# Kernel optimization log

Measured on AMD Instinct MI355X. Metric: run time of the kernel, lower is better.

## Reference

```python
import jax, jax.numpy as jnp
import numpy as np

B, S, V, H, L, NH, DH, F = 1, 512, 30522, 768, 12, 12, 64, 3072
N, E, GH, NC = 50000, 800000, 128, 3


def setup_inputs() -> dict:
    key = jax.random.key(0)
    ks = iter(jax.random.split(key, 48))
    def nrm(shape, s=0.02):
        return jax.random.normal(next(ks), shape, jnp.float32) * s
    inp = {
        "input_ids": jax.random.randint(next(ks), (B, S), 0, V, dtype=jnp.int32),
        "attention_mask": jnp.ones((B, S), jnp.int32),
        "token_type_ids": jnp.zeros((B, S), jnp.int32),
        "premise_edge_index": jax.random.randint(next(ks), (2, E), 0, N, dtype=jnp.int32),
        "hypothesis_edge_index": jax.random.randint(next(ks), (2, E), 0, N, dtype=jnp.int32),
        "premise_node_features": nrm((N, H), 1.0),
        "hypothesis_node_features": nrm((N, H), 1.0),
        "word_emb": nrm((V, H)), "pos_emb": nrm((S, H)), "type_emb": nrm((2, H)),
        "emb_ln_s": jnp.ones((H,)), "emb_ln_b": jnp.zeros((H,)),
        "Wq": nrm((L, H, H)), "bq": jnp.zeros((L, H)),
        "Wk": nrm((L, H, H)), "bk": jnp.zeros((L, H)),
        "Wv": nrm((L, H, H)), "bv": jnp.zeros((L, H)),
        "Wo": nrm((L, H, H)), "bo": jnp.zeros((L, H)),
        "ln1_s": jnp.ones((L, H)), "ln1_b": jnp.zeros((L, H)),
        "W1": nrm((L, H, F)), "b1": jnp.zeros((L, F)),
        "W2": nrm((L, F, H)), "b2": jnp.zeros((L, H)),
        "ln2_s": jnp.ones((L, H)), "ln2_b": jnp.zeros((L, H)),
        "gcn_W1": nrm((H, GH), 0.05), "gcn_b1": jnp.zeros((GH,)),
        "gcn_W2": nrm((GH, GH), 0.05), "gcn_b2": jnp.zeros((GH,)),
        "comb_W": nrm((2 * (H + GH), H)), "comb_b": jnp.zeros((H,)),
        "cls_W": nrm((H, NC)), "cls_b": jnp.zeros((NC,)),
    }
    return inp


def _ln(x, s, b, eps=1e-12):
    m = jnp.mean(x, -1, keepdims=True)
    v = jnp.mean(jnp.square(x - m), -1, keepdims=True)
    return (x - m) * jax.lax.rsqrt(v + eps) * s + b


def _gcn(x, edge_index, W1, b1, W2, b2):
    # PyG GCNConv: add self-loops, symmetric D^-1/2 A D^-1/2 normalization,
    # linear transform first, then scatter-add messages at destination.
    n = x.shape[0]
    loops = jnp.arange(n, dtype=edge_index.dtype)
    src = jnp.concatenate([edge_index[0], loops])
    dst = jnp.concatenate([edge_index[1], loops])
    deg = jax.ops.segment_sum(jnp.ones(src.shape[0], jnp.float32), dst, num_segments=n)
    dinv = jnp.where(deg > 0, jax.lax.rsqrt(jnp.maximum(deg, 1e-12)), 0.0)
    norm = (dinv[src] * dinv[dst])[:, None]
    def conv(h, W, b):
        hw = h @ W
        return jax.ops.segment_sum(hw[src] * norm, dst, num_segments=n) + b
    h = jax.nn.relu(conv(x, W1, b1))
    h = conv(h, W2, b2)
    # global_mean_pool with batch=None -> single graph mean, shape [1, GH]
    return jnp.mean(h, axis=0, keepdims=True)


def _bert(input_ids, attention_mask, token_type_ids, word_emb, pos_emb, type_emb, emb_ln_s, emb_ln_b, layer_params):
    s = input_ids.shape[1]
    h = word_emb[input_ids] + pos_emb[None, :s] + type_emb[token_type_ids]
    h = _ln(h, emb_ln_s, emb_ln_b)
    bias = (1.0 - attention_mask.astype(jnp.float32))[:, None, None, :] * -1e4
    def step(h, p):
        wq, bq, wk, bk, wv, bv, wo, bo, l1s, l1b, w1, b1_, w2, b2_, l2s, l2b = p
        b_, s_, _ = h.shape
        q = (h @ wq + bq).reshape(b_, s_, NH, DH)
        k = (h @ wk + bk).reshape(b_, s_, NH, DH)
        v = (h @ wv + bv).reshape(b_, s_, NH, DH)
        scores = jnp.einsum('bqhd,bkhd->bhqk', q, k) / np.float32(np.sqrt(DH)) + bias
        ctx = jnp.einsum('bhqk,bkhd->bqhd', jax.nn.softmax(scores, -1), v).reshape(b_, s_, H)
        h1 = _ln(h + ctx @ wo + bo, l1s, l1b)
        f = jax.nn.gelu(h1 @ w1 + b1_, approximate=False) @ w2 + b2_
        return _ln(h1 + f, l2s, l2b), None
    h, _ = jax.lax.scan(step, h, layer_params)
    return h[:, 0, :]  # CLS pooling, [B, H]


def reference(input_ids, attention_mask, token_type_ids, premise_edge_index, premise_node_features, hypothesis_edge_index, hypothesis_node_features, word_emb, pos_emb, type_emb, emb_ln_s, emb_ln_b, Wq, bq, Wk, bk, Wv, bv, Wo, bo, ln1_s, ln1_b, W1, b1, W2, b2, ln2_s, ln2_b, gcn_W1, gcn_b1, gcn_W2, gcn_b2, comb_W, comb_b, cls_W, cls_b):
    lp = (Wq, bq, Wk, bk, Wv, bv, Wo, bo, ln1_s, ln1_b, W1, b1, W2, b2, ln2_s, ln2_b)
    cls = _bert(input_ids, attention_mask, token_type_ids, word_emb, pos_emb, type_emb, emb_ln_s, emb_ln_b, lp)
    gp = _gcn(premise_node_features, premise_edge_index, gcn_W1, gcn_b1, gcn_W2, gcn_b2)
    gh = _gcn(hypothesis_node_features, hypothesis_edge_index, gcn_W1, gcn_b1, gcn_W2, gcn_b2)
    cp = jnp.concatenate([cls, gp], -1)
    ch = jnp.concatenate([cls, gh], -1)
    fc = jnp.concatenate([cp, ch], -1)  # [1, 2*(H+GH)]
    feat = jax.nn.relu(fc @ comb_W + comb_b)  # dropout is identity at eval
    return feat @ cls_W + cls_b
```

## Files before the change

kernel.cpp:

```cpp
#include <hip/hip_runtime.h>
#include <math.h>

constexpr int kS = 512, kH = 768, kNH = 12, kDH = 64, kF = 3072, kL = 12;
constexpr int kN = 50000, kE = 800000, kGH = 128;

#define CDIV(a,b) (((a)+(b)-1)/(b))

struct Ptr3 { const float* p[3]; };

typedef __attribute__((ext_vector_type(8))) short bf16x8;
typedef __attribute__((ext_vector_type(4))) float f32x4;

__device__ __forceinline__ unsigned short bf16_rne(float f) {
    unsigned int u = __float_as_uint(f);
    u += 0x7fffu + ((u >> 16) & 1u);
    return (unsigned short)(u >> 16);
}
__device__ __forceinline__ float bf16_f32(unsigned short h) {
    return __uint_as_float(((unsigned int)h) << 16);
}
__device__ __forceinline__ void split2(float f, short& hi, short& lo) {
    unsigned short h = bf16_rne(f);
    hi = (short)h;
    lo = (short)bf16_rne(f - bf16_f32(h));
// ... 122 lines not shown
        for (int j = 0; j < 4; j++) acc[i][j] = (f32x4){0.f, 0.f, 0.f, 0.f};
    int nst = Kc / 32;
    bf16x8 pa0 = *(const bf16x8*)(Agh);
    bf16x8 pa1 = *(const bf16x8*)(Agl);
    bf16x8 pb0 = *(const bf16x8*)(Bgh);
    bf16x8 pb1 = *(const bf16x8*)(Bgh + 8);
    bf16x8 pb2 = *(const bf16x8*)(Bgl);
    bf16x8 pb3 = *(const bf16x8*)(Bgl + 8);
    for (int st = 0; st < nst; ++st) {
        *(bf16x8*)&As[aofs]      = pa0;
        *(bf16x8*)&As[aofs + 32] = pa1;
        *(bf16x8*)&Bs[bofs]      = pb0;
        *(bf16x8*)&Bs[bofs + 8]  = pb1;
        *(bf16x8*)&Bs[bofs + 32] = pb2;
        *(bf16x8*)&Bs[bofs + 40] = pb3;
        if (st + 1 < nst) {
            int go = (st + 1) * 32;
            pa0 = *(const bf16x8*)(Agh + go);
            pa1 = *(const bf16x8*)(Agl + go);
            pb0 = *(const bf16x8*)(Bgh + go);
            pb1 = *(const bf16x8*)(Bgh + go + 8);
            pb2 = *(const bf16x8*)(Bgl + go);
            pb3 = *(const bf16x8*)(Bgl + go + 8);
        }
        __syncthreads();
        bf16x8 bh[4], bl[4];
        #pragma unroll
        for (int j = 0; j < 4; j++) {
            int c = (wn + j * 16 + fr) * LDR + ko;
            bh[j] = *(const bf16x8*)&Bs[c];
            bl[j] = *(const bf16x8*)&Bs[c + 32];
        }
        #pragma unroll
        for (int i = 0; i < 2; i++) {
            int r = (wm + i * 16 + fr) * LDR + ko;
            bf16x8 ah = *(const bf16x8*)&As[r];
            bf16x8 al = *(const bf16x8*)&As[r + 32];
            #pragma unroll
            for (int j = 0; j < 4; j++) {
                acc[i][j] = __builtin_amdgcn_mfma_f32_16x16x32_bf16(ah, bh[j], acc[i][j], 0, 0, 0);
                acc[i][j] = __builtin_amdgcn_mfma_f32_16x16x32_bf16(ah, bl[j], acc[i][j], 0, 0, 0);
                acc[i][j] = __builtin_amdgcn_mfma_f32_16x16x32_bf16(al, bh[j], acc[i][j], 0, 0, 0);
            }
        }
        __syncthreads();
    }
    long MN = (long)M * Nn;
    float* Pp = part + (long)(w * S + s) * MN;
    int cr = (lane >> 4) * 4;
    #pragma unroll
    for (int i = 0; i < 2; i++) {
        #pragma unroll
        for (int r = 0; r < 4; r++) {
            int gm = m0 + wm + i * 16 + cr + r;
            float* rowp = &Pp[(long)gm * Nn + n0 + wn + fr];
            #pragma unroll
            for (int j = 0; j < 4; j++) rowp[j * 16] = acc[i][j][r];
        }
    }
}

__global__ __launch_bounds__(256, 4) void gemm64_gcn(
    const float* __restrict__ A,
    const short* __restrict__ Bth, const short* __restrict__ Btl,
    float* __restrict__ part, int M, int Nn, int K, int S)
{
    __shared__ short As[64 * LDR], Bs[128 * LDR];
    int s = blockIdx.z;
    int Kc = K / S, kbeg = s * Kc;
    int m0 = blockIdx.y * 64, n0 = blockIdx.x * 128;
    int tid = threadIdx.x;
    int ar = tid >> 2, aqf = (tid & 3) * 8;
    int gmA = m0 + ar; if (gmA > M - 1) gmA = M - 1;
    const float* Agf = A + (long)gmA * K + kbeg + aqf;
    int aofs = ar * LDR + aqf;
    int br = tid >> 1, bq = (tid & 1) * 16;
    const short* Bgh = Bth + (long)(n0 + br) * K + kbeg + bq;
    const short* Bgl = Btl + (long)(n0 + br) * K + kbeg + bq;
    int bofs = br * LDR + bq;
    int wid = tid >> 6, lane = tid & 63;
    int wm = (wid >> 1) * 32, wn = (wid & 1) * 64;
    int fr = lane & 15, ko = (lane >> 4) * 8;
    f32x4 acc[2][4];
    #pragma unroll
    for (int i = 0; i < 2; i++)
        #pragma unroll
        for (int j = 0; j < 4; j++) acc[i][j] = (f32x4){0.f, 0.f, 0.f, 0.f};
    int nst = Kc / 32;
    float4 pf0 = *(const float4*)(Agf);
    float4 pf1 = *(const float4*)(Agf + 4);
    bf16x8 pb0 = *(const bf16x8*)(Bgh);
    bf16x8 pb1 = *(const bf16x8*)(Bgh + 8);
    bf16x8 pb2 = *(const bf16x8*)(Bgl);
    bf16x8 pb3 = *(const bf16x8*)(Bgl + 8);
    for (int st = 0; st < nst; ++st) {
        short h0, l0, h1, l1, h2, l2, h3, l3, h4, l4, h5, l5, h6, l6, h7, l7;
        split2(pf0.x, h0, l0); split2(pf0.y, h1, l1); split2(pf0.z, h2, l2); split2(pf0.w, h3, l3);
        split2(pf1.x, h4, l4); split2(pf1.y, h5, l5); split2(pf1.z, h6, l6); split2(pf1.w, h7, l7);
        *(short4*)&As[aofs]      = make_short4(h0, h1, h2, h3);
        *(short4*)&As[aofs + 4]  = make_short4(h4, h5, h6, h7);
        *(short4*)&As[aofs + 32] = make_short4(l0, l1, l2, l3);
        *(short4*)&As[aofs + 36] = make_short4(l4, l5, l6, l7);
        *(bf16x8*)&Bs[bofs]      = pb0;
        *(bf16x8*)&Bs[bofs + 8]  = pb1;
        *(bf16x8*)&Bs[bofs + 32] = pb2;
        *(bf16x8*)&Bs[bofs + 40] = pb3;
        if (st + 1 < nst) {
            int go = (st + 1) * 32;
            pf0 = *(const float4*)(Agf + go);
            pf1 = *(const float4*)(Agf + go + 4);
            pb0 = *(const bf16x8*)(Bgh + go);
            pb1 = *(const bf16x8*)(Bgh + go + 8);
            pb2 = *(const bf16x8*)(Bgl + go);
            pb3 = *(const bf16x8*)(Bgl + go + 8);
        }
        __syncthreads();
        bf16x8 bh[4], bl[4];
        #pragma unroll
        for (int j = 0; j < 4; j++) {
            int c = (wn + j * 16 + fr) * LDR + ko;
            bh[j] = *(const bf16x8*)&Bs[c];
            bl[j] = *(const bf16x8*)&Bs[c + 32];
        }
        #pragma unroll
        for (int i = 0; i < 2; i++) {
            int r = (wm + i * 16 + fr) * LDR + ko;
            bf16x8 ah = *(const bf16x8*)&As[r];
            bf16x8 al = *(const bf16x8*)&As[r + 32];
            #pragma unroll
            for (int j = 0; j < 4; j++) {
                acc[i][j] = __builtin_amdgcn_mfma_f32_16x16x32_bf16(ah, bh[j], acc[i][j], 0, 0, 0);
                acc[i][j] = __builtin_amdgcn_mfma_f32_16x16x32_bf16(ah, bl[j], acc[i][j], 0, 0, 0);
                acc[i][j] = __builtin_amdgcn_mfma_f32_16x16x32_bf16(al, bh[j], acc[i][j], 0, 0, 0);
            }
        }
        __syncthreads();
    }
    long MN = (long)M * Nn;
    float* Pp = part + (long)s * MN;
    int cr = (lane >> 4) * 4;
    #pragma unroll
    for (int i = 0; i < 2; i++) {
        #pragma unroll
        for (int r = 0; r < 4; r++) {
            int gm = m0 + wm + i * 16 + cr + r;
            if (gm >= M) continue;
            float* rowp = &Pp[(long)gm * Nn + n0 + wn + fr];
            #pragma unroll
            for (int j = 0; j < 4; j++) rowp[j * 16] = acc[i][j][r];
        }
    }
}

__global__ void splitk_epi_qkv_kernel(const float* __restrict__ part, Ptr3 bias,
                                      short* __restrict__ qh, short* __restrict__ ql,
                                      short* __restrict__ kh, short* __restrict__ kl,
                                      short* __restrict__ vh, short* __restrict__ vl,
                                      int S) {
    const long MN = (long)kS * kH;
    int w = blockIdx.y;
    long i = ((long)blockIdx.x * blockDim.x + threadIdx.x) * 4;
    if (i >= MN) return;
    const float* P = part + (long)w * S * MN + i;
    float4 a = *(const float4*)P;
    for (int s2 = 1; s2 < S; ++s2) {
        float4 b2 = *(const float4*)(P + (long)s2 * MN);
        a.x += b2.x; a.y += b2.y; a.z += b2.z; a.w += b2.w;
    }
    const float* bw = bias.p[w];
    int n = (int)(i % kH);
    a.x += bw[n]; a.y += bw[n + 1]; a.z += bw[n + 2]; a.w += bw[n + 3];
    short* oh = (w == 0) ? qh : (w == 1) ? kh : vh;
    short* ol = (w == 0) ? ql : (w == 1) ? kl : vl;
    short h0, l0, h1, l1, h2, l2, h3, l3;
    split2(a.x, h0, l0); split2(a.y, h1, l1); split2(a.z, h2, l2); split2(a.w, h3, l3);
    *(short4*)&oh[i] = make_short4(h0, h1, h2, h3);
    *(short4*)&ol[i] = make_short4(l0, l1, l2, l3);
}

__global__ void splitk_epi_sh_kernel(const float* __restrict__ part, const float* __restrict__ bias,
                                     short* __restrict__ oh, short* __restrict__ ol,
                                     long MN, int Nn, int S, int act) {
    long i = ((long)blockIdx.x * blockDim.x + threadIdx.x) * 4;
    if (i >= MN) return;
    const float* P = part + i;
    float4 a = *(const float4*)P;
    for (int s2 = 1; s2 < S; ++s2) {
        float4 b2 = *(const float4*)(P + (long)s2 * MN);
        a.x += b2.x; a.y += b2.y; a.z += b2.z; a.w += b2.w;
    }
    if (bias) {
        int n = (int)(i % Nn);
        a.x += bias[n]; a.y += bias[n + 1]; a.z += bias[n + 2]; a.w += bias[n + 3];
    }
    if (act == 1) {
        a.x = 0.5f * a.x * (1.f + erff(a.x * 0.70710678118654752f));
        a.y = 0.5f * a.y * (1.f + erff(a.y * 0.70710678118654752f));
        a.z = 0.5f * a.z * (1.f + erff(a.z * 0.70710678118654752f));
        a.w = 0.5f * a.w * (1.f + erff(a.w * 0.70710678118654752f));
    }
    short h0, l0, h1, l1, h2, l2, h3, l3;
    split2(a.x, h0, l0); split2(a.y, h1, l1); split2(a.z, h2, l2); split2(a.w, h3, l3);
    *(short4*)&oh[i] = make_short4(h0, h1, h2, h3);
    *(short4*)&ol[i] = make_short4(l0, l1, l2, l3);
}

__global__ void splitk_epi_ln2_kernel(const float* __restrict__ part, const float* __restrict__ bias,
                                      const float* __restrict__ res, const float* __restrict__ g,
                                      const float* __restrict__ b, float* __restrict__ out,
                                      short* __restrict__ oh, short* __restrict__ ol, int S) {
    int row = blockIdx.x; int tid = threadIdx.x;
    __shared__ float red[256];
    const long MN = (long)kS * kH;
    float vals[3]; float sum = 0.f;
    #pragma unroll
    for (int r = 0; r < 3; r++) {
        int j = tid + r * 256;
        const float* P = part + (long)row * kH + j;
        float x = res[(long)row * kH + j] + bias[j];
        for (int s2 = 0; s2 < S; ++s2) x += P[(long)s2 * MN];
        vals[r] = x; sum += x;
    }
    red[tid] = sum; __syncthreads();
    for (int off = 128; off > 0; off >>= 1) { if (tid < off) red[tid] += red[tid + off]; __syncthreads(); }
    float mean = red[0] / kH; __syncthreads();
    float vs = 0.f;
    #pragma unroll
    for (int r = 0; r < 3; r++) { float d = vals[r] - mean; vs += d * d; }
    red[tid] = vs; __syncthreads();
    for (int off = 128; off > 0; off >>= 1) { if (tid < off) red[tid] += red[tid + off]; __syncthreads(); }
    float rstd = rsqrtf(red[0] / kH + 1e-12f);
    #pragma unroll
    for (int r = 0; r < 3; r++) {
        int j = tid + r * 256;
        float o = (vals[r] - mean) * rstd * g[j] + b[j];
        out[(long)row * kH + j] = o;
        short hi, lo; split2(o, hi, lo);
        oh[(long)row * kH + j] = hi; ol[(long)row * kH + j] = lo;
    }
}

__global__ __launch_bounds__(256, 4) void attn_scores64_kernel(
    const short* __restrict__ qh, const short* __restrict__ ql,
    const short* __restrict__ kh, const short* __restrict__ kl,
    const float* __restrict__ mb, float* __restrict__ scores)
{
    __shared__ short As[64 * LDR], Bs[128 * LDR];
    int h = blockIdx.z;
    int k0 = blockIdx.x * 128, q0 = blockIdx.y * 64;
    int tid = threadIdx.x;
    int ar = tid >> 2, aq = (tid & 3) * 8;
    const short* Agh = qh + (long)(q0 + ar) * kH + h * kDH + aq;
    const short* Agl = ql + (long)(q0 + ar) * kH + h * kDH + aq;
    int aofs = ar * LDR + aq;
    int br = tid >> 1, bq = (tid & 1) * 16;
    const short* Bgh = kh + (long)(k0 + br) * kH + h * kDH + bq;
    const short* Bgl = kl + (long)(k0 + br) * kH + h * kDH + bq;
    int bofs = br * LDR + bq;
    int wid = tid >> 6, lane = tid & 63;
    int wm = (wid >> 1) * 32, wn = (wid & 1) * 64;
    int fr = lane & 15, ko = (lane >> 4) * 8;
    f32x4 acc[2][4];
    #pragma unroll
    for (int i = 0; i < 2; i++)
        #pragma unroll
        for (int j = 0; j < 4; j++) acc[i][j] = (f32x4){0.f, 0.f, 0.f, 0.f};
    bf16x8 pa0 = *(const bf16x8*)(Agh);
    bf16x8 pa1 = *(const bf16x8*)(Agl);
    bf16x8 pb0 = *(const bf16x8*)(Bgh);
    bf16x8 pb1 = *(const bf16x8*)(Bgh + 8);
    bf16x8 pb2 = *(const bf16x8*)(Bgl);
    bf16x8 pb3 = *(const bf16x8*)(Bgl + 8);
    #pragma unroll
    for (int st = 0; st < 2; ++st) {
        *(bf16x8*)&As[aofs]      = pa0;
        *(bf16x8*)&As[aofs + 32] = pa1;
        *(bf16x8*)&Bs[bofs]      = pb0;
        *(bf16x8*)&Bs[bofs + 8]  = pb1;
        *(bf16x8*)&Bs[bofs + 32] = pb2;
        *(bf16x8*)&Bs[bofs + 40] = pb3;
        if (st == 0) {
            pa0 = *(const bf16x8*)(Agh + 32);
            pa1 = *(const bf16x8*)(Agl + 32);
            pb0 = *(const bf16x8*)(Bgh + 32);
            pb1 = *(const bf16x8*)(Bgh + 40);
            pb2 = *(const bf16x8*)(Bgl + 32);
            pb3 = *(const bf16x8*)(Bgl + 40);
        }
        __syncthreads();
        bf16x8 bh[4], bl[4];
        #pragma unroll
        for (int j = 0; j < 4; j++) {
            int c = (wn + j * 16 + fr) * LDR + ko;
            bh[j] = *(const bf16x8*)&Bs[c];
            bl[j] = *(const bf16x8*)&Bs[c + 32];
        }
        #pragma unroll
        for (int i = 0; i < 2; i++) {
            int r = (wm + i * 16 + fr) * LDR + ko;
            bf16x8 ah = *(const bf16x8*)&As[r];
            bf16x8 al = *(const bf16x8*)&As[r + 32];
            #pragma unroll
            for (int j = 0; j < 4; j++) {
                acc[i][j] = __builtin_amdgcn_mfma_f32_16x16x32_bf16(ah, bh[j], acc[i][j], 0, 0, 0);
                acc[i][j] = __builtin_amdgcn_mfma_f32_16x16x32_bf16(ah, bl[j], acc[i][j], 0, 0, 0);
                acc[i][j] = __builtin_amdgcn_mfma_f32_16x16x32_bf16(al, bh[j], acc[i][j], 0, 0, 0);
            }
        }
        __syncthreads();
    }
    int cr = (lane >> 4) * 4;
    #pragma unroll
    for (int i = 0; i < 2; i++) {
        #pragma unroll
        for (int r = 0; r < 4; r++) {
            int qq = q0 + wm + i * 16 + cr + r;
            float* rowp = &scores[((long)h * kS + qq) * kS + k0 + wn + fr];
            #pragma unroll
            for (int j = 0; j < 4; j++)
                rowp[j * 16] = acc[i][j][r] * 0.125f + mb[k0 + wn + j * 16 + fr];
        }
    }
}

__global__ void softmax_split_kernel(const float* __restrict__ scores,
                                     short* __restrict__ ph, short* __restrict__ pl) {
    long row = blockIdx.x;
    const float* p = scores + row * kS;
    int tid = threadIdx.x;
    __shared__ float red[256];
    float x0 = p[tid], x1 = p[tid + 256];
    red[tid] = fmaxf(x0, x1); __syncthreads();
    for (int off = 128; off > 0; off >>= 1) { if (tid < off) red[tid] = fmaxf(red[tid], red[tid + off]); __syncthreads(); }
    float mx = red[0]; __syncthreads();
    float e0 = expf(x0 - mx), e1 = expf(x1 - mx);
    red[tid] = e0 + e1; __syncthreads();
    for (int off = 128; off > 0; off >>= 1) { if (tid < off) red[tid] += red[tid + off]; __syncthreads(); }
    float inv = 1.f / red[0];
    float r0 = e0 * inv, r1 = e1 * inv;
    short h0, l0, h1, l1;
    split2(r0, h0, l0); split2(r1, h1, l1);
    ph[row * kS + tid] = h0; pl[row * kS + tid] = l0;
    ph[row * kS + tid + 256] = h1; pl[row * kS + tid + 256] = l1;
}

__global__ __launch_bounds__(256, 4) void attn_ctx64_kernel(
    const short* __restrict__ ph, const short* __restrict__ pl,
    const short* __restrict__ vth, const short* __restrict__ vtl,
    float* __restrict__ part)
{
    __shared__ short As[128 * LDR], Bs[64 * LDR];
    int q0 = blockIdx.x * 128;
    int h = blockIdx.y >> 3, s = blockIdx.y & 7;
    int kbeg = s * 64;
    int tid = threadIdx.x;
    int ar = tid >> 1, aq = (tid & 1) * 16;
    const short* Agh = ph + ((long)h * kS + q0 + ar) * kS + kbeg + aq;
    const short* Agl = pl + ((long)h * kS + q0 + ar) * kS + kbeg + aq;
    int aofs = ar * LDR + aq;
    int brr = tid >> 2, bq = (tid & 3) * 8;
    const short* Bgh = vth + ((long)h * kDH + brr) * kS + kbeg + bq;
    const short* Bgl = vtl + ((long)h * kDH + brr) * kS + kbeg + bq;
    int bofs = brr * LDR + bq;
    int wid = tid >> 6, lane = tid & 63;
    int wm = wid * 32;
    int fr = lane & 15, ko = (lane >> 4) * 8;
    f32x4 acc[2][4];
    #pragma unroll
    for (int i = 0; i < 2; i++)
        #pragma unroll
        for (int j = 0; j < 4; j++) acc[i][j] = (f32x4){0.f, 0.f, 0.f, 0.f};
    bf16x8 pa0 = *(const bf16x8*)(Agh);
    bf16x8 pa1 = *(const bf16x8*)(Agh + 8);
    bf16x8 pa2 = *(const bf16x8*)(Agl);
    bf16x8 pa3 = *(const bf16x8*)(Agl + 8);
    bf16x8 pb0 = *(const bf16x8*)(Bgh);
    bf16x8 pb1 = *(const bf16x8*)(Bgl);
    #pragma unroll
    for (int st = 0; st < 2; ++st) {
        *(bf16x8*)&As[aofs]      = pa0;
        *(bf16x8*)&As[aofs + 8]  = pa1;
        *(bf16x8*)&As[aofs + 32] = pa2;
        *(bf16x8*)&As[aofs + 40] = pa3;
        *(bf16x8*)&Bs[bofs]      = pb0;
        *(bf16x8*)&Bs[bofs + 32] = pb1;
        if (st == 0) {
            pa0 = *(const bf16x8*)(Agh + 32);
            pa1 = *(const bf16x8*)(Agh + 40);
            pa2 = *(const bf16x8*)(Agl + 32);
            pa3 = *(const bf16x8*)(Agl + 40);
            pb0 = *(const bf16x8*)(Bgh + 32);
            pb1 = *(const bf16x8*)(Bgl + 32);
        }
        __syncthreads();
        bf16x8 bh[4], bl[4];
        #pragma unroll
        for (int j = 0; j < 4; j++) {
            int c = (j * 16 + fr) * LDR + ko;
            bh[j] = *(const bf16x8*)&Bs[c];
            bl[j] = *(const bf16x8*)&Bs[c + 32];
        }
        #pragma unroll
        for (int i = 0; i < 2; i++) {
            int r = (wm + i * 16 + fr) * LDR + ko;
            bf16x8 ah = *(const bf16x8*)&As[r];
            bf16x8 al = *(const bf16x8*)&As[r + 32];
            #pragma unroll
            for (int j = 0; j < 4; j++) {
                acc[i][j] = __builtin_amdgcn_mfma_f32_16x16x32_bf16(ah, bh[j], acc[i][j], 0, 0, 0);
                acc[i][j] = __builtin_amdgcn_mfma_f32_16x16x32_bf16(ah, bl[j], acc[i][j], 0, 0, 0);
                acc[i][j] = __builtin_amdgcn_mfma_f32_16x16x32_bf16(al, bh[j], acc[i][j], 0, 0, 0);
            }
        }
        __syncthreads();
    }
    long Pbase = (long)s * ((long)kS * kH);
    int cr = (lane >> 4) * 4;
    #pragma unroll
    for (int i = 0; i < 2; i++) {
        #pragma unroll
        for (int r = 0; r < 4; r++) {
            int gq = q0 + wm + i * 16 + cr + r;
            float* rowp = &part[Pbase + (long)gq * kH + h * kDH + fr];
            #pragma unroll
            for (int j = 0; j < 4; j++) rowp[j * 16] = acc[i][j][r];
        }
    }
}

__global__ void cnt_kernel(const int* __restrict__ dst, int* __restrict__ cnt, int E) {
    int e = blockIdx.x * blockDim.x + threadIdx.x;
    if (e < E) atomicAdd(&cnt[dst[e]], 1);
}

__global__ void scan1_kernel(const int* __restrict__ cnt, int* __restrict__ offs,
                             int* __restrict__ bsum, int n) {
    __shared__ int sh[256];
    int i = blockIdx.x * 256 + threadIdx.x;
    int v = (i < n) ? cnt[i] : 0;
    sh[threadIdx.x] = v; __syncthreads();
    for (int off = 1; off < 256; off <<= 1) {
        int t = (threadIdx.x >= off) ? sh[threadIdx.x - off] : 0;
        __syncthreads();
        sh[threadIdx.x] += t;
        __syncthreads();
    }
    if (i < n) offs[i] = sh[threadIdx.x] - v;
    if (threadIdx.x == 255) bsum[blockIdx.x] = sh[255];
}

__global__ void scan2_kernel(int* bsum, int nb, int* offs, int n) {
    if (threadIdx.x == 0) {
        int run = 0;
        for (int b = 0; b < nb; b++) { int t = bsum[b]; bsum[b] = run; run += t; }
        offs[n] = run;
    }
}

__global__ void scan3_kernel(const int* __restrict__ cnt, int* __restrict__ offs,
                             const int* __restrict__ bsum, int* __restrict__ cur,
                             float* __restrict__ dinv, int n) {
    int i = blockIdx.x * 256 + threadIdx.x;
    if (i >= n) return;
    int o = offs[i] + bsum[blockIdx.x];
    offs[i] = o; cur[i] = o;
    dinv[i] = rsqrtf((float)(cnt[i] + 1));
}

__global__ void csrfill_edgew_kernel(const int* __restrict__ src, const int* __restrict__ dst,
                                     int* __restrict__ cur, int* __restrict__ csr,
                                     const float* __restrict__ dinv, float* __restrict__ wsum,
                                     int E) {
    int e = blockIdx.x * blockDim.x + threadIdx.x;
    if (e < E) {
        int s2 = src[e], d = dst[e];
        int slot = atomicAdd(&cur[d], 1);
        csr[slot] = s2;
        atomicAdd(&wsum[s2], dinv[s2] * dinv[d]);
    }
}

__global__ __launch_bounds__(256) void spmm_gather_kernel(const int* __restrict__ offs,
                                                          const int* __restrict__ csr,
                                                          const float* __restrict__ dinv,
                                                          const float* __restrict__ hw,
                                                          const float* __restrict__ b1,
                                                          float* __restrict__ hout, int n) {
    int d = blockIdx.x * 2 + (threadIdx.x >> 7);
    int j = threadIdx.x & 127;
    if (d >= n) return;
    int beg = offs[d], end = offs[d + 1];
    float a0 = 0.f, a1 = 0.f, a2 = 0.f, a3 = 0.f;
    int p = beg;
    for (; p + 4 <= end; p += 4) {
        int s0 = csr[p], s1 = csr[p + 1], s2 = csr[p + 2], s3 = csr[p + 3];
        a0 += dinv[s0] * hw[(long)s0 * kGH + j];
        a1 += dinv[s1] * hw[(long)s1 * kGH + j];
        a2 += dinv[s2] * hw[(long)s2 * kGH + j];
        a3 += dinv[s3] * hw[(long)s3 * kGH + j];
    }
    for (; p < end; ++p) {
        int s4 = csr[p];
        a0 += dinv[s4] * hw[(long)s4 * kGH + j];
    }
    float acc = (a0 + a1) + (a2 + a3);
    float dd = dinv[d];
    float v = acc * dd + dd * dd * hw[(long)d * kGH + j] + b1[j];
    hout[(long)d * kGH + j] = fmaxf(v, 0.f);
}

__global__ void wreduce_kernel(const float* __restrict__ h, const float* __restrict__ w,
                               const float* __restrict__ dinv, float* __restrict__ s, int n) {
    int tid = threadIdx.x; int j = tid & 127; int half = tid >> 7;
    float acc = 0.f;
    for (int u = blockIdx.x * 2 + half; u < n; u += gridDim.x * 2) {
        float di = dinv[u];
        acc += (w[u] + di * di) * h[(long)u * kGH + j];
    }
    __shared__ float red[256];
    red[tid] = acc; __syncthreads();
    if (tid < 128) atomicAdd(&s[j], red[tid] + red[tid + 128]);
}

__global__ void gcn_final_kernel(const float* s, const float* W2, const float* b2, float* g) {
    int j2 = threadIdx.x;
    float acc = 0.f;
    for (int j = 0; j < kGH; j++) acc += s[j] * W2[(long)j * kGH + j2];
    g[j2] = acc * (1.f / (float)kN) + b2[j2];
}

__global__ void combine_part_kernel(const float* __restrict__ cls, const float* __restrict__ gp,
                                    const float* __restrict__ gh, const float* __restrict__ Wc,
                                    float* __restrict__ feat) {
    int i0 = blockIdx.x * 32;
    int tid = threadIdx.x;
    float a0 = 0.f, a1 = 0.f, a2 = 0.f;
    for (int r = 0; r < 32; r++) {
        int i = i0 + r;
        float x = (i < 768) ? cls[i] : (i < 896) ? gp[i - 768]
                : (i < 1664) ? cls[i - 896] : gh[i - 1664];
        const float* row = Wc + (long)i * kH;
        a0 += x * row[tid]; a1 += x * row[tid + 256]; a2 += x * row[tid + 512];
    }
    atomicAdd(&feat[tid], a0);
    atomicAdd(&feat[tid + 256], a1);
    atomicAdd(&feat[tid + 512], a2);
}

__global__ void combine_fin_kernel(float* feat, const float* bc) {
    int o = blockIdx.x * 256 + threadIdx.x;
    if (o < kH) feat[o] = fmaxf(feat[o] + bc[o], 0.f);
}

__global__ void cls_head_kernel(const float* feat, const float* W, const float* b, float* out) {
    int tid = threadIdx.x;
    float a0 = 0.f, a1 = 0.f, a2 = 0.f;
    for (int o = tid; o < kH; o += 256) {
        float f = feat[o];
        a0 += f * W[o * 3 + 0]; a1 += f * W[o * 3 + 1]; a2 += f * W[o * 3 + 2];
    }
    __shared__ float r0[256], r1[256], r2[256];
    r0[tid] = a0; r1[tid] = a1; r2[tid] = a2; __syncthreads();
    for (int off = 128; off > 0; off >>= 1) {
        if (tid < off) { r0[tid] += r0[tid + off]; r1[tid] += r1[tid + off]; r2[tid] += r2[tid + off]; }
        __syncthreads();
    }
    if (tid == 0) { out[0] = r0[0] + b[0]; out[1] = r1[0] + b[1]; out[2] = r2[0] + b[2]; }
}

extern "C" void kernel_launch(void* const* d_in, const int* in_sizes, int n_in,
                              void* d_out, int out_size, void* d_ws, size_t ws_size,
                              hipStream_t stream) {
    const int*   input_ids = (const int*)d_in[0];
    const int*   attn_mask = (const int*)d_in[1];
    const int*   type_ids  = (const int*)d_in[2];
    const int*   p_edges   = (const int*)d_in[3];
    const int*   h_edges   = (const int*)d_in[4];
    const float* p_nodes   = (const float*)d_in[5];
    const float* h_nodes   = (const float*)d_in[6];
    const float* word_emb  = (const float*)d_in[7];
    const float* pos_emb   = (const float*)d_in[8];
    const float* type_emb  = (const float*)d_in[9];
    const float* eln_s     = (const float*)d_in[10];
    const float* eln_b     = (const float*)d_in[11];
    const float* Wq = (const float*)d_in[12]; const float* bq = (const float*)d_in[13];
    const float* Wk = (const float*)d_in[14]; const float* bk = (const float*)d_in[15];
    const float* Wv = (const float*)d_in[16]; const float* bv = (const float*)d_in[17];
    const float* Wo = (const float*)d_in[18]; const float* bo = (const float*)d_in[19];
    const float* l1s = (const float*)d_in[20]; const float* l1b = (const float*)d_in[21];
    const float* W1 = (const float*)d_in[22]; const float* b1 = (const float*)d_in[23];
    const float* W2 = (const float*)d_in[24]; const float* b2 = (const float*)d_in[25];
    const float* l2s = (const float*)d_in[26]; const float* l2b = (const float*)d_in[27];
    const float* gW1 = (const float*)d_in[28]; const float* gb1 = (const float*)d_in[29];
    const float* gW2 = (const float*)d_in[30]; const float* gb2 = (const float*)d_in[31];
    const float* cW  = (const float*)d_in[32]; const float* cb  = (const float*)d_in[33];
    const float* clsW = (const float*)d_in[34]; const float* clsB = (const float*)d_in[35];
    float* out = (float*)d_out;

    float* W = (float*)d_ws;
    size_t off = 0;
    auto alloc = [&](size_t n) { float* p = W + off; off += n; return p; };
    float* h    = alloc((size_t)kS * kH);
    float* h1   = alloc((size_t)kS * kH);
    float* deg  = alloc(kN);
    float* wsum = alloc(kN);
    float* svec = alloc(kGH);
    float* gp   = alloc(kGH);
    float* ghv  = alloc(kGH);
    float* mb   = alloc(kS);
    float* feat = alloc(kH);
    float* big  = W + off;

    float* part  = big;
    float* scores = part;
    short* p_h   = (short*)(big + 4718592);
    short* p_l   = p_h + (size_t)3145728;
    short* ffn1_h = (short*)(big + 7864320);
    short* ffn1_l = ffn1_h + (size_t)1572864;
    short* sm    = (short*)(big + 11796480);
    const size_t SMN = (size_t)kS * kH;
    short* q_h = sm;            short* q_l = q_h + SMN;
    short* k_h = q_l + SMN;     short* k_l = k_h + SMN;
    short* v_h = k_l + SMN;     short* v_l = v_h + SMN;
    short* vt_h = v_l + SMN;    short* vt_l = vt_h + SMN;
    short* ctx_h = vt_l + SMN;  short* ctx_l = ctx_h + SMN;
    short* h1_h = ctx_l + SMN;  short* h1_l = h1_h + SMN;
    short* hh_h = h1_l + SMN;   short* hh_l = hh_h + SMN;

    float* hw1 = big;
    float* agg = big + (size_t)kN * kGH;
    int* icnt  = (int*)(big + 2 * (size_t)kN * kGH);
    int* ioffs = icnt + 50048;
    int* icur  = ioffs + 50048;
    int* ibsum = icur + 50048;
    int* icsr  = ibsum + 256;
    short* gwt_h = (short*)(icsr + kE);
    short* gwt_l = gwt_h + (size_t)kH * kGH;

    const size_t QKV_SZ = (size_t)kH * kH;
    const size_t FF_SZ  = (size_t)kH * kF;
    short* wc = (short*)(big + 15000000);
    short* qkv_h = wc;                          short* qkv_l = qkv_h + 12 * 3 * QKV_SZ;
    short* wo_h  = qkv_l + 12 * 3 * QKV_SZ;     short* wo_l  = wo_h + 12 * QKV_SZ;
    short* w1_h  = wo_l + 12 * QKV_SZ;          short* w1_l  = w1_h + 12 * FF_SZ;
    short* w2_h  = w1_l + 12 * FF_SZ;           short* w2_l  = w2_h + 12 * FF_SZ;

    const long MN_H = (long)kS * kH;
    const long MN_F = (long)kS * kF;
    const int nScanBlk = CDIV(kN, 256);

    wtrans_all_kernel<<<dim3(24, 24, 12), 256, 0, stream>>>(Wq, qkv_h,              qkv_l,              kH, kH, (long)(3 * QKV_SZ));
    wtrans_all_kernel<<<dim3(24, 24, 12), 256, 0, stream>>>(Wk, qkv_h + QKV_SZ,     qkv_l + QKV_SZ,     kH, kH, (long)(3 * QKV_SZ));
    wtrans_all_kernel<<<dim3(24, 24, 12), 256, 0, stream>>>(Wv, qkv_h + 2 * QKV_SZ, qkv_l + 2 * QKV_SZ, kH, kH, (long)(3 * QKV_SZ));
    wtrans_all_kernel<<<dim3(24, 24, 12), 256, 0, stream>>>(Wo, wo_h, wo_l, kH, kH, (long)QKV_SZ);
    wtrans_all_kernel<<<dim3(96, 24, 12), 256, 0, stream>>>(W1, w1_h, w1_l, kH, kF, (long)FF_SZ);
    wtrans_all_kernel<<<dim3(24, 96, 12), 256, 0, stream>>>(W2, w2_h, w2_l, kF, kH, (long)FF_SZ);

    const int* gsrc[2] = { p_edges, h_edges };
    const int* gdst[2] = { p_edges + kE, h_edges + kE };
    const float* gx[2] = { p_nodes, h_nodes };
    float* gout[2] = { gp, ghv };
    wtrans_all_kernel<<<dim3(kGH / 32, kH / 32, 1), 256, 0, stream>>>(gW1, gwt_h, gwt_l, kH, kGH, 0);
    for (int gi = 0; gi < 2; gi++) {
        gcn_zero_kernel<<<nScanBlk, 256, 0, stream>>>(icnt, wsum, svec);
        cnt_kernel<<<CDIV(kE, 256), 256, 0, stream>>>(gdst[gi], icnt, kE);
        scan1_kernel<<<nScanBlk, 256, 0, stream>>>(icnt, ioffs, ibsum, kN);
        scan2_kernel<<<1, 64, 0, stream>>>(ibsum, nScanBlk, ioffs, kN);
        scan3_kernel<<<nScanBlk, 256, 0, stream>>>(icnt, ioffs, ibsum, icur, deg, kN);
        csrfill_edgew_kernel<<<CDIV(kE, 256), 256, 0, stream>>>(
            gsrc[gi], gdst[gi], icur, icsr, deg, wsum, kE);
        gemm64_gcn<<<dim3(1, CDIV(kN, 64), 1), 256, 0, stream>>>(
            gx[gi], gwt_h, gwt_l, hw1, kN, kGH, kH, 1);
        spmm_gather_kernel<<<CDIV(kN, 2), 256, 0, stream>>>(ioffs, icsr, deg, hw1, gb1, agg, kN);
        wreduce_kernel<<<512, 256, 0, stream>>>(agg, wsum, deg, svec, kN);
        gcn_final_kernel<<<1, kGH, 0, stream>>>(svec, gW2, gb2, gout[gi]);
    }

    embed_ln_kernel<<<kS, 256, 0, stream>>>(input_ids, type_ids, attn_mask,
                                            word_emb, pos_emb, type_emb,
                                            eln_s, eln_b, h, hh_h, hh_l, mb);
    for (int l = 0; l < kL; l++) {
        const float* bq_l = bq + (size_t)l * kH;
        const float* bk_l = bk + (size_t)l * kH;
        const float* bv_l = bv + (size_t)l * kH;
        const float* bo_l = bo + (size_t)l * kH;
        const float* b1_l = b1 + (size_t)l * kF;
        const float* b2_l = b2 + (size_t)l * kH;
        const float* l1s_l = l1s + (size_t)l * kH; const float* l1b_l = l1b + (size_t)l * kH;
        const float* l2s_l = l2s + (size_t)l * kH; const float* l2b_l = l2b + (size_t)l * kH;
        const short* qkvh_l = qkv_h + (size_t)l * 3 * QKV_SZ;
        const short* qkvl_l = qkv_l + (size_t)l * 3 * QKV_SZ;
        const short* woh_l = wo_h + (size_t)l * QKV_SZ;
        const short* wol_l = wo_l + (size_t)l * QKV_SZ;
        const short* w1h_l = w1_h + (size_t)l * FF_SZ;
        const short* w1l_l = w1_l + (size_t)l * FF_SZ;
        const short* w2h_l = w2_h + (size_t)l * FF_SZ;
        const short* w2l_l = w2_l + (size_t)l * FF_SZ;

        gemm64_pre<<<dim3(kH / 128, kS / 64, 12), 256, 0, stream>>>(
            hh_h, hh_l, qkvh_l, qkvl_l, (long)QKV_SZ, part, kS, kH, kH, 4);
        splitk_epi_qkv_kernel<<<dim3((int)(MN_H / 4 / 256), 3), 256, 0, stream>>>(
            part, Ptr3{{bq_l, bk_l, bv_l}}, q_h, q_l, k_h, k_l, v_h, v_l, 4);
        vtrans_kernel<<<dim3(kS / 32, kNH * 2), 256, 0, stream>>>(v_h, v_l, vt_h, vt_l);
        attn_scores64_kernel<<<dim3(kS / 128, kS / 64, kNH), 256, 0, stream>>>(
            q_h, q_l, k_h, k_l, mb, scores);
        softmax_split_kernel<<<kNH * kS, 256, 0, stream>>>(scores, p_h, p_l);
        attn_ctx64_kernel<<<dim3(kS / 128, kNH * 8), 256, 0, stream>>>(p_h, p_l, vt_h, vt_l, part);
        splitk_epi_sh_kernel<<<(int)(MN_H / 4 / 256), 256, 0, stream>>>(
            part, nullptr, ctx_h, ctx_l, MN_H, kH, 8, 0);
        gemm64_pre<<<dim3(kH / 128, kS / 64, 8), 256, 0, stream>>>(
            ctx_h, ctx_l, woh_l, wol_l, 0, part, kS, kH, kH, 8);
        splitk_epi_ln2_kernel<<<kS, 256, 0, stream>>>(part, bo_l, h, l1s_l, l1b_l, h1, h1_h, h1_l, 8);
        gemm64_pre<<<dim3(kF / 128, kS / 64, 4), 256, 0, stream>>>(
            h1_h, h1_l, w1h_l, w1l_l, 0, part, kS, kF, kH, 4);
        splitk_epi_sh_kernel<<<(int)(MN_F / 4 / 256), 256, 0, stream>>>(
            part, b1_l, ffn1_h, ffn1_l, MN_F, kF, 4, 1);
        gemm64_pre<<<dim3(kH / 128, kS / 64, 8), 256, 0, stream>>>(
            ffn1_h, ffn1_l, w2h_l, w2l_l, 0, part, kS, kH, kF, 8);
        splitk_epi_ln2_kernel<<<kS, 256, 0, stream>>>(part, b2_l, h1, l2s_l, l2b_l, h, hh_h, hh_l, 8);
    }

    fill_kernel<<<3, 256, 0, stream>>>(feat, 0.f, kH);
    combine_part_kernel<<<56, 256, 0, stream>>>(h, gp, ghv, cW, feat);
    combine_fin_kernel<<<3, 256, 0, stream>>>(feat, cb);
    cls_head_kernel<<<1, 256, 0, stream>>>(feat, clsW, clsB, out);
}
```

Before: 2.454 ms.

## Fuse attention scores, softmax, and context into one flash-attention kernel

Replaces the separate score GEMM, softmax, context GEMM and split-K epilogue with a single online-softmax flash attention kernel per 64-query tile and head. This removes the fp32 score buffer and the split bf16 probability buffers and their round trips through global memory, plus three launches per layer. The cost is a small grid (96 blocks of 128 threads), serialized K/V tile loads with many barriers, and a sequential split of the unnormalized probabilities into hi and lo passes, which can leave the GPU underused. Separately, the GCN aggregation loop is unrolled from 4 to 8 accumulators to expose more memory-level parallelism.

```diff
diff --git a/kernel.cpp b/kernel.cpp
--- a/kernel.cpp
+++ b/kernel.cpp
@@ -298,6 +298,219 @@
     }
 }
 
+__global__ __launch_bounds__(128) void flash_attn_kernel(
+    const short* __restrict__ qh, const short* __restrict__ ql,
+    const short* __restrict__ kh, const short* __restrict__ kl,
+    const short* __restrict__ vth, const short* __restrict__ vtl,
+    const float* __restrict__ mb,
+    short* __restrict__ ctxh, short* __restrict__ ctxl)
+{
+    __shared__ short Qs[2 * 64 * LDR];
+    __shared__ short Ks[128 * LDR];
+    __shared__ short Ps[4 * 64 * 40];
+    int h = blockIdx.y;
+    int q0 = blockIdx.x * 64;
+    int tid = threadIdx.x;
+    int wid = tid >> 6, lane = tid & 63;
+    int wm = wid * 32;
+    int fr = lane & 15, ko = (lane >> 4) * 8;
+    int cr4 = (lane >> 4) * 4;
+    {
+        int row = tid >> 1, dseg = tid & 1;
+        const short* gh_ = qh + (long)(q0 + row) * kH + h * kDH + dseg * 32;
+        const short* gl_ = ql + (long)(q0 + row) * kH + h * kDH + dseg * 32;
+        short* dst = &Qs[(dseg * 64 + row) * LDR];
+        #pragma unroll
+        for (int c = 0; c < 4; c++) {
+            *(bf16x8*)&dst[c * 8]      = *(const bf16x8*)(gh_ + c * 8);
+            *(bf16x8*)&dst[32 + c * 8] = *(const bf16x8*)(gl_ + c * 8);
+        }
+    }
+    float mrun[2][4], lrun[2][4];
+    f32x4 accO[2][4];
+    #pragma unroll
+    for (int i = 0; i < 2; i++)
+        #pragma unroll
+        for (int r = 0; r < 4; r++) { mrun[i][r] = -1e30f; lrun[i][r] = 0.f; }
+    #pragma unroll
+    for (int i = 0; i < 2; i++)
+        #pragma unroll
+        for (int j = 0; j < 4; j++) accO[i][j] = (f32x4){0.f, 0.f, 0.f, 0.f};
+
+    for (int t = 0; t < 4; ++t) {
+        int k0t = t * 128;
+        f32x4 accS[2][8];
+        #pragma unroll
+        for (int i = 0; i < 2; i++)
+            #pragma unroll
+            for (int j = 0; j < 8; j++) accS[i][j] = (f32x4){0.f, 0.f, 0.f, 0.f};
+        for (int st = 0; st < 2; ++st) {
+            __syncthreads();
+            {
+                int row = tid;
+                const short* gh_ = kh + (long)(k0t + row) * kH + h * kDH + st * 32;
+                const short* gl_ = kl + (long)(k0t + row) * kH + h * kDH + st * 32;
+                short* dst = &Ks[row * LDR];
+                #pragma unroll
+                for (int c = 0; c < 4; c++) {
+                    *(bf16x8*)&dst[c * 8]      = *(const bf16x8*)(gh_ + c * 8);
+                    *(bf16x8*)&dst[32 + c * 8] = *(const bf16x8*)(gl_ + c * 8);
+                }
+            }
+            __syncthreads();
+            bf16x8 bh[8], bl[8];
+            #pragma unroll
+            for (int j = 0; j < 8; j++) {
+                int c = (j * 16 + fr) * LDR + ko;
+                bh[j] = *(const bf16x8*)&Ks[c];
+                bl[j] = *(const bf16x8*)&Ks[c + 32];
+            }
+            #pragma unroll
+            for (int i = 0; i < 2; i++) {
+                int r = (st * 64 + wm + i * 16 + fr) * LDR + ko;
+                bf16x8 ah = *(const bf16x8*)&Qs[r];
+                bf16x8 al = *(const bf16x8*)&Qs[r + 32];
+                #pragma unroll
+                for (int j = 0; j < 8; j++) {
+                    accS[i][j] = __builtin_amdgcn_mfma_f32_16x16x32_bf16(ah, bh[j], accS[i][j], 0, 0, 0);
+                    accS[i][j] = __builtin_amdgcn_mfma_f32_16x16x32_bf16(ah, bl[j], accS[i][j], 0, 0, 0);
+                    accS[i][j] = __builtin_amdgcn_mfma_f32_16x16x32_bf16(al, bh[j], accS[i][j], 0, 0, 0);
+                }
+            }
+        }
+        float mbv[8];
+        #pragma unroll
+        for (int j = 0; j < 8; j++) mbv[j] = mb[k0t + j * 16 + fr];
+        #pragma unroll
+        for (int i = 0; i < 2; i++) {
+            #pragma unroll
+            for (int r = 0; r < 4; r++) {
+                float mt = -1e30f;
+                #pragma unroll
+                for (int j = 0; j < 8; j++) {
+                    float sv = accS[i][j][r] * 0.125f + mbv[j];
+                    accS[i][j][r] = sv;
+                    mt = fmaxf(mt, sv);
+                }
+                #pragma unroll
+                for (int mmask = 1; mmask < 16; mmask <<= 1)
+                    mt = fmaxf(mt, __shfl_xor(mt, mmask, 64));
+                float mn = fmaxf(mrun[i][r], mt);
+                float sc = __expf(mrun[i][r] - mn);
+                mrun[i][r] = mn;
+                lrun[i][r] *= sc;
+                #pragma unroll
+                for (int jo = 0; jo < 4; jo++) {
+                    accO[i][jo][r] *= sc;
+                }
+                float lt = 0.f;
+                #pragma unroll
+                for (int j = 0; j < 8; j++) {
+                    float p = __expf(accS[i][j][r] - mn);
+                    accS[i][j][r] = p;
+                    lt += p;
+                }
+                #pragma unroll
+                for (int mmask = 1; mmask < 16; mmask <<= 1)
+                    lt += __shfl_xor(lt, mmask, 64);
+                lrun[i][r] += lt;
+            }
+        }
+        #pragma unroll
+        for (int i = 0; i < 2; i++)
+            #pragma unroll
+            for (int j = 0; j < 8; j++)
+                #pragma unroll
+                for (int r = 0; r < 4; r++) {
+                    int rowp = wm + i * 16 + cr4 + r;
+                    Ps[(j >> 1) * 2560 + rowp * 40 + (j & 1) * 16 + fr] =
+                        (short)bf16_rne(accS[i][j][r]);
+                }
+        for (int st2 = 0; st2 < 4; ++st2) {
+            __syncthreads();
+            {
+                int row = tid >> 1, half = tid & 1;
+                const short* gh_ = vth + ((long)h * kDH + row) * kS + k0t + st2 * 32 + half * 16;
+                const short* gl_ = vtl + ((long)h * kDH + row) * kS + k0t + st2 * 32 + half * 16;
+                short* dst = &Ks[row * LDR + half * 16];
+                *(bf16x8*)&dst[0]  = *(const bf16x8*)(gh_);
+                *(bf16x8*)&dst[8]  = *(const bf16x8*)(gh_ + 8);
+                *(bf16x8*)&dst[32] = *(const bf16x8*)(gl_);
+                *(bf16x8*)&dst[40] = *(const bf16x8*)(gl_ + 8);
+            }
+            __syncthreads();
+            bf16x8 vh_[4], vl_[4];
+            #pragma unroll
+            for (int j = 0; j < 4; j++) {
+                int c = (j * 16 + fr) * LDR + ko;
+                vh_[j] = *(const bf16x8*)&Ks[c];
+                vl_[j] = *(const bf16x8*)&Ks[c + 32];
+            }
+            #pragma unroll
+            for (int i = 0; i < 2; i++) {
+                bf16x8 pa = *(const bf16x8*)&Ps[st2 * 2560 + (wm + i * 16 + fr) * 40 + ko];
+                #pragma unroll
+                for (int j = 0; j < 4; j++) {
+                    accO[i][j] = __builtin_amdgcn_mfma_f32_16x16x32_bf16(pa, vh_[j], accO[i][j], 0, 0, 0);
+                    accO[i][j] = __builtin_amdgcn_mfma_f32_16x16x32_bf16(pa, vl_[j], accO[i][j], 0, 0, 0);
+                }
+            }
+        }
+        __syncthreads();
+        #pragma unroll
+        for (int i = 0; i < 2; i++)
+            #pragma unroll
+            for (int j = 0; j < 8; j++)
+                #pragma unroll
+                for (int r = 0; r < 4; r++) {
+                    int rowp = wm + i * 16 + cr4 + r;
+                    float p = accS[i][j][r];
+                    unsigned short ph = bf16_rne(p);
+                    Ps[(j >> 1) * 2560 + rowp * 40 + (j & 1) * 16 + fr] =
+                        (short)bf16_rne(p - bf16_f32(ph));
+                }
+        for (int st2 = 0; st2 < 4; ++st2) {
+            __syncthreads();
+            {
+                int row = tid >> 1, half = tid & 1;
+                const short* gh_ = vth + ((long)h * kDH + row) * kS + k0t + st2 * 32 + half * 16;
+                short* dst = &Ks[row * LDR + half * 16];
+                *(bf16x8*)&dst[0] = *(const bf16x8*)(gh_);
+                *(bf16x8*)&dst[8] = *(const bf16x8*)(gh_ + 8);
+            }
+            __syncthreads();
+            bf16x8 vh_[4];
+            #pragma unroll
+            for (int j = 0; j < 4; j++)
+                vh_[j] = *(const bf16x8*)&Ks[(j * 16 + fr) * LDR + ko];
+            #pragma unroll
+            for (int i = 0; i < 2; i++) {
+                bf16x8 pa = *(const bf16x8*)&Ps[st2 * 2560 + (wm + i * 16 + fr) * 40 + ko];
+                #pragma unroll
+                for (int j = 0; j < 4; j++)
+                    accO[i][j] = __builtin_amdgcn_mfma_f32_16x16x32_bf16(pa, vh_[j], accO[i][j], 0, 0, 0);
+            }
+        }
+        __syncthreads();
+    }
+    #pragma unroll
+    for (int i = 0; i < 2; i++) {
+        #pragma unroll
+        for (int r = 0; r < 4; r++) {
+            float inv = 1.f / lrun[i][r];
+            int q = q0 + wm + i * 16 + cr4 + r;
+            #pragma unroll
+            for (int j = 0; j < 4; j++) {
+                float o = accO[i][j][r] * inv;
+                int col = h * kDH + j * 16 + fr;
+                short hi, lo; split2(o, hi, lo);
+                ctxh[(long)q * kH + col] = hi;
+                ctxl[(long)q * kH + col] = lo;
+            }
+        }
+    }
+}
+
 __global__ void splitk_epi_qkv_kernel(const float* __restrict__ part, Ptr3 bias,
                                       short* __restrict__ qh, short* __restrict__ ql,
                                       short* __restrict__ kh, short* __restrict__ kl,
@@ -386,194 +599,6 @@
     }
 }
 
-__global__ __launch_bounds__(256, 4) void attn_scores64_kernel(
-    const short* __restrict__ qh, const short* __restrict__ ql,
-    const short* __restrict__ kh, const short* __restrict__ kl,
-    const float* __restrict__ mb, float* __restrict__ scores)
-{
-    __shared__ short As[64 * LDR], Bs[128 * LDR];
-    int h = blockIdx.z;
-    int k0 = blockIdx.x * 128, q0 = blockIdx.y * 64;
-    int tid = threadIdx.x;
-    int ar = tid >> 2, aq = (tid & 3) * 8;
-    const short* Agh = qh + (long)(q0 + ar) * kH + h * kDH + aq;
-    const short* Agl = ql + (long)(q0 + ar) * kH + h * kDH + aq;
-    int aofs = ar * LDR + aq;
-    int br = tid >> 1, bq = (tid & 1) * 16;
-    const short* Bgh = kh + (long)(k0 + br) * kH + h * kDH + bq;
-    const short* Bgl = kl + (long)(k0 + br) * kH + h * kDH + bq;
-    int bofs = br * LDR + bq;
-    int wid = tid >> 6, lane = tid & 63;
-    int wm = (wid >> 1) * 32, wn = (wid & 1) * 64;
-    int fr = lane & 15, ko = (lane >> 4) * 8;
-    f32x4 acc[2][4];
-    #pragma unroll
-    for (int i = 0; i < 2; i++)
-        #pragma unroll
-        for (int j = 0; j < 4; j++) acc[i][j] = (f32x4){0.f, 0.f, 0.f, 0.f};
-    bf16x8 pa0 = *(const bf16x8*)(Agh);
-    bf16x8 pa1 = *(const bf16x8*)(Agl);
-    bf16x8 pb0 = *(const bf16x8*)(Bgh);
-    bf16x8 pb1 = *(const bf16x8*)(Bgh + 8);
-    bf16x8 pb2 = *(const bf16x8*)(Bgl);
-    bf16x8 pb3 = *(const bf16x8*)(Bgl + 8);
-    #pragma unroll
-    for (int st = 0; st < 2; ++st) {
-        *(bf16x8*)&As[aofs]      = pa0;
-        *(bf16x8*)&As[aofs + 32] = pa1;
-        *(bf16x8*)&Bs[bofs]      = pb0;
-        *(bf16x8*)&Bs[bofs + 8]  = pb1;
-        *(bf16x8*)&Bs[bofs + 32] = pb2;
-        *(bf16x8*)&Bs[bofs + 40] = pb3;
-        if (st == 0) {
-            pa0 = *(const bf16x8*)(Agh + 32);
-            pa1 = *(const bf16x8*)(Agl + 32);
-            pb0 = *(const bf16x8*)(Bgh + 32);
-            pb1 = *(const bf16x8*)(Bgh + 40);
-            pb2 = *(const bf16x8*)(Bgl + 32);
-            pb3 = *(const bf16x8*)(Bgl + 40);
-        }
-        __syncthreads();
-        bf16x8 bh[4], bl[4];
-        #pragma unroll
-        for (int j = 0; j < 4; j++) {
-            int c = (wn + j * 16 + fr) * LDR + ko;
-            bh[j] = *(const bf16x8*)&Bs[c];
-            bl[j] = *(const bf16x8*)&Bs[c + 32];
-        }
-        #pragma unroll
-        for (int i = 0; i < 2; i++) {
-            int r = (wm + i * 16 + fr) * LDR + ko;
-            bf16x8 ah = *(const bf16x8*)&As[r];
-            bf16x8 al = *(const bf16x8*)&As[r + 32];
-            #pragma unroll
-            for (int j = 0; j < 4; j++) {
-                acc[i][j] = __builtin_amdgcn_mfma_f32_16x16x32_bf16(ah, bh[j], acc[i][j], 0, 0, 0);
-                acc[i][j] = __builtin_amdgcn_mfma_f32_16x16x32_bf16(ah, bl[j], acc[i][j], 0, 0, 0);
-                acc[i][j] = __builtin_amdgcn_mfma_f32_16x16x32_bf16(al, bh[j], acc[i][j], 0, 0, 0);
-            }
-        }
-        __syncthreads();
-    }
-    int cr = (lane >> 4) * 4;
-    #pragma unroll
-    for (int i = 0; i < 2; i++) {
-        #pragma unroll
-        for (int r = 0; r < 4; r++) {
-            int qq = q0 + wm + i * 16 + cr + r;
-            float* rowp = &scores[((long)h * kS + qq) * kS + k0 + wn + fr];
-            #pragma unroll
-            for (int j = 0; j < 4; j++)
-                rowp[j * 16] = acc[i][j][r] * 0.125f + mb[k0 + wn + j * 16 + fr];
-        }
-    }
-}
-
-__global__ void softmax_split_kernel(const float* __restrict__ scores,
-                                     short* __restrict__ ph, short* __restrict__ pl) {
-    long row = blockIdx.x;
-    const float* p = scores + row * kS;
-    int tid = threadIdx.x;
-    __shared__ float red[256];
-    float x0 = p[tid], x1 = p[tid + 256];
-    red[tid] = fmaxf(x0, x1); __syncthreads();
-    for (int off = 128; off > 0; off >>= 1) { if (tid < off) red[tid] = fmaxf(red[tid], red[tid + off]); __syncthreads(); }
-    float mx = red[0]; __syncthreads();
-    float e0 = expf(x0 - mx), e1 = expf(x1 - mx);
-    red[tid] = e0 + e1; __syncthreads();
-    for (int off = 128; off > 0; off >>= 1) { if (tid < off) red[tid] += red[tid + off]; __syncthreads(); }
-    float inv = 1.f / red[0];
-    float r0 = e0 * inv, r1 = e1 * inv;
-    short h0, l0, h1, l1;
-    split2(r0, h0, l0); split2(r1, h1, l1);
-    ph[row * kS + tid] = h0; pl[row * kS + tid] = l0;
-    ph[row * kS + tid + 256] = h1; pl[row * kS + tid + 256] = l1;
-}
-
-__global__ __launch_bounds__(256, 4) void attn_ctx64_kernel(
-    const short* __restrict__ ph, const short* __restrict__ pl,
-    const short* __restrict__ vth, const short* __restrict__ vtl,
-    float* __restrict__ part)
-{
-    __shared__ short As[128 * LDR], Bs[64 * LDR];
-    int q0 = blockIdx.x * 128;
-    int h = blockIdx.y >> 3, s = blockIdx.y & 7;
-    int kbeg = s * 64;
-    int tid = threadIdx.x;
-    int ar = tid >> 1, aq = (tid & 1) * 16;
-    const short* Agh = ph + ((long)h * kS + q0 + ar) * kS + kbeg + aq;
-    const short* Agl = pl + ((long)h * kS + q0 + ar) * kS + kbeg + aq;
-    int aofs = ar * LDR + aq;
-    int brr = tid >> 2, bq = (tid & 3) * 8;
-    const short* Bgh = vth + ((long)h * kDH + brr) * kS + kbeg + bq;
-    const short* Bgl = vtl + ((long)h * kDH + brr) * kS + kbeg + bq;
-    int bofs = brr * LDR + bq;
-    int wid = tid >> 6, lane = tid & 63;
-    int wm = wid * 32;
-    int fr = lane & 15, ko = (lane >> 4) * 8;
-    f32x4 acc[2][4];
-    #pragma unroll
-    for (int i = 0; i < 2; i++)
-        #pragma unroll
-        for (int j = 0; j < 4; j++) acc[i][j] = (f32x4){0.f, 0.f, 0.f, 0.f};
-    bf16x8 pa0 = *(const bf16x8*)(Agh);
-    bf16x8 pa1 = *(const bf16x8*)(Agh + 8);
-    bf16x8 pa2 = *(const bf16x8*)(Agl);
-    bf16x8 pa3 = *(const bf16x8*)(Agl + 8);
-    bf16x8 pb0 = *(const bf16x8*)(Bgh);
-    bf16x8 pb1 = *(const bf16x8*)(Bgl);
-    #pragma unroll
-    for (int st = 0; st < 2; ++st) {
-        *(bf16x8*)&As[aofs]      = pa0;
-        *(bf16x8*)&As[aofs + 8]  = pa1;
-        *(bf16x8*)&As[aofs + 32] = pa2;
-        *(bf16x8*)&As[aofs + 40] = pa3;
-        *(bf16x8*)&Bs[bofs]      = pb0;
-        *(bf16x8*)&Bs[bofs + 32] = pb1;
-        if (st == 0) {
-            pa0 = *(const bf16x8*)(Agh + 32);
-            pa1 = *(const bf16x8*)(Agh + 40);
-            pa2 = *(const bf16x8*)(Agl + 32);
-            pa3 = *(const bf16x8*)(Agl + 40);
-            pb0 = *(const bf16x8*)(Bgh + 32);
-            pb1 = *(const bf16x8*)(Bgl + 32);
-        }
-        __syncthreads();
-        bf16x8 bh[4], bl[4];
-        #pragma unroll
-        for (int j = 0; j < 4; j++) {
-            int c = (j * 16 + fr) * LDR + ko;
-            bh[j] = *(const bf16x8*)&Bs[c];
-            bl[j] = *(const bf16x8*)&Bs[c + 32];
-        }
-        #pragma unroll
-        for (int i = 0; i < 2; i++) {
-            int r = (wm + i * 16 + fr) * LDR + ko;
-            bf16x8 ah = *(const bf16x8*)&As[r];
-            bf16x8 al = *(const bf16x8*)&As[r + 32];
-            #pragma unroll
-            for (int j = 0; j < 4; j++) {
-                acc[i][j] = __builtin_amdgcn_mfma_f32_16x16x32_bf16(ah, bh[j], acc[i][j], 0, 0, 0);
-                acc[i][j] = __builtin_amdgcn_mfma_f32_16x16x32_bf16(ah, bl[j], acc[i][j], 0, 0, 0);
-                acc[i][j] = __builtin_amdgcn_mfma_f32_16x16x32_bf16(al, bh[j], acc[i][j], 0, 0, 0);
-            }
-        }
-        __syncthreads();
-    }
-    long Pbase = (long)s * ((long)kS * kH);
-    int cr = (lane >> 4) * 4;
-    #pragma unroll
-    for (int i = 0; i < 2; i++) {
-        #pragma unroll
-        for (int r = 0; r < 4; r++) {
-            int gq = q0 + wm + i * 16 + cr + r;
-            float* rowp = &part[Pbase + (long)gq * kH + h * kDH + fr];
-            #pragma unroll
-            for (int j = 0; j < 4; j++) rowp[j * 16] = acc[i][j][r];
-        }
-    }
-}
-
 __global__ void cnt_kernel(const int* __restrict__ dst, int* __restrict__ cnt, int E) {
     int e = blockIdx.x * blockDim.x + threadIdx.x;
     if (e < E) atomicAdd(&cnt[dst[e]], 1);
@@ -637,19 +662,25 @@
     if (d >= n) return;
     int beg = offs[d], end = offs[d + 1];
     float a0 = 0.f, a1 = 0.f, a2 = 0.f, a3 = 0.f;
+    float a4 = 0.f, a5 = 0.f, a6 = 0.f, a7 = 0.f;
     int p = beg;
-    for (; p + 4 <= end; p += 4) {
+    for (; p + 8 <= end; p += 8) {
         int s0 = csr[p], s1 = csr[p + 1], s2 = csr[p + 2], s3 = csr[p + 3];
+        int s4 = csr[p + 4], s5 = csr[p + 5], s6 = csr[p + 6], s7 = csr[p + 7];
         a0 += dinv[s0] * hw[(long)s0 * kGH + j];
         a1 += dinv[s1] * hw[(long)s1 * kGH + j];
         a2 += dinv[s2] * hw[(long)s2 * kGH + j];
         a3 += dinv[s3] * hw[(long)s3 * kGH + j];
+        a4 += dinv[s4] * hw[(long)s4 * kGH + j];
+        a5 += dinv[s5] * hw[(long)s5 * kGH + j];
+        a6 += dinv[s6] * hw[(long)s6 * kGH + j];
+        a7 += dinv[s7] * hw[(long)s7 * kGH + j];
     }
     for (; p < end; ++p) {
-        int s4 = csr[p];
-        a0 += dinv[s4] * hw[(long)s4 * kGH + j];
-    }
-    float acc = (a0 + a1) + (a2 + a3);
+        int s8 = csr[p];
+        a0 += dinv[s8] * hw[(long)s8 * kGH + j];
+    }
+    float acc = ((a0 + a1) + (a2 + a3)) + ((a4 + a5) + (a6 + a7));
     float dd = dinv[d];
     float v = acc * dd + dd * dd * hw[(long)d * kGH + j] + b1[j];
     hout[(long)d * kGH + j] = fmaxf(v, 0.f);
@@ -758,9 +789,6 @@
     float* big  = W + off;
 
     float* part  = big;
-    float* scores = part;
-    short* p_h   = (short*)(big + 4718592);
-    short* p_l   = p_h + (size_t)3145728;
     short* ffn1_h = (short*)(big + 7864320);
     short* ffn1_l = ffn1_h + (size_t)1572864;
     short* sm    = (short*)(big + 11796480);
@@ -848,12 +876,8 @@
         splitk_epi_qkv_kernel<<<dim3((int)(MN_H / 4 / 256), 3), 256, 0, stream>>>(
             part, Ptr3{{bq_l, bk_l, bv_l}}, q_h, q_l, k_h, k_l, v_h, v_l, 4);
         vtrans_kernel<<<dim3(kS / 32, kNH * 2), 256, 0, stream>>>(v_h, v_l, vt_h, vt_l);
-        attn_scores64_kernel<<<dim3(kS / 128, kS / 64, kNH), 256, 0, stream>>>(
-            q_h, q_l, k_h, k_l, mb, scores);
-        softmax_split_kernel<<<kNH * kS, 256, 0, stream>>>(scores, p_h, p_l);
-        attn_ctx64_kernel<<<dim3(kS / 128, kNH * 8), 256, 0, stream>>>(p_h, p_l, vt_h, vt_l, part);
-        splitk_epi_sh_kernel<<<(int)(MN_H / 4 / 256), 256, 0, stream>>>(
-            part, nullptr, ctx_h, ctx_l, MN_H, kH, 8, 0);
+        flash_attn_kernel<<<dim3(kS / 64, kNH), 128, 0, stream>>>(
+            q_h, q_l, k_h, k_l, vt_h, vt_l, mb, ctx_h, ctx_l);
         gemm64_pre<<<dim3(kH / 128, kS / 64, 8), 256, 0, stream>>>(
             ctx_h, ctx_l, woh_l, wol_l, 0, part, kS, kH, kH, 8);
         splitk_epi_ln2_kernel<<<kS, 256, 0, stream>>>(part, bo_l, h, l1s_l, l1b_l, h1, h1_h, h1_l, 8);
```

After: 2.418 ms. No clear change (-1.4%).
